# Performance work log

Hardware: AMD Instinct MI355X
Metric: run time of the kernel (lower is better)

## Reference

```python
import jax, jax.numpy as jnp
import numpy as np

T, B, D = 128, 64, 1024  # timesteps, batch, mem_dim (== in_dim)


def setup_inputs() -> dict:
    key = jax.random.key(0)
    ks = jax.random.split(key, 10)
    w = lambda k, shape: jax.random.normal(k, shape, dtype=jnp.float32) * 0.02
    return dict(
        c=jax.random.normal(ks[0], (T, B, D), dtype=jnp.float32),
        q=jax.random.normal(ks[1], (B, D), dtype=jnp.float32),
        Wb_w=w(ks[2], (D, D)),                 # nn.Linear(mem_dim, mem_dim, bias=False)
        W1_w=w(ks[3], (D, 9 * D)),             # nn.Linear(9*mem_dim, mem_dim)
        W1_b=jnp.zeros((D,), jnp.float32),
        W2_w=w(ks[4], (D, D)),                 # nn.Linear(mem_dim, mem_dim)
        W2_b=jnp.zeros((D,), jnp.float32),
        mem_Wih=w(ks[5], (3 * D, D)), mem_Whh=w(ks[6], (3 * D, D)),
        mem_bih=jnp.zeros((3 * D,), jnp.float32), mem_bhh=jnp.zeros((3 * D,), jnp.float32),
        att_Wih=w(ks[7], (3 * D, D)), att_Whh=w(ks[8], (3 * D, D)),
        att_bih=jnp.zeros((3 * D,), jnp.float32), att_bhh=jnp.zeros((3 * D,), jnp.float32),
    )


def gru_cell(x, h, Wih, Whh, bih, bhh):
    # torch.nn.GRUCell semantics
    gi = x @ Wih.T + bih  # [B, 3D]
    gh = h @ Whh.T + bhh  # [B, 3D]
    i_r, i_z, i_n = jnp.split(gi, 3, axis=-1)
    h_r, h_z, h_n = jnp.split(gh, 3, axis=-1)
    r = jax.nn.sigmoid(i_r + h_r)
    z = jax.nn.sigmoid(i_z + h_z)
    n = jnp.tanh(i_n + r * h_n)
    return (1.0 - z) * n + z * h


def reference(c, q, Wb_w, W1_w, W1_b, W2_w, W2_b,
              mem_Wih, mem_Whh, mem_bih, mem_bhh,
              att_Wih, att_Whh, att_bih, att_bhh):
    N_EPISODE = 2

    def episode(m):
        # Wb(q), Wb(m) are step-invariant -> hoist out of the scan
        Wbq = q @ Wb_w.T  # [B, D]
        Wbm = m @ Wb_w.T  # [B, D]

        def step(h, c_t):
            # make_z: 9-way feature concat -> [B, 9D]
            z = jnp.concatenate(
                [c_t, m, q, c_t * q, c_t * m,
                 jnp.abs(c_t - q), jnp.abs(c_t - m),
                 c_t * Wbq, c_t * Wbm], axis=-1)
            g1 = jnp.tanh(z @ W1_w.T + W1_b)            # [B, D]
            g = jax.nn.sigmoid(g1 @ W2_w.T + W2_b)      # [B, D]
            h_att = gru_cell(c_t, h, att_Wih, att_Whh, att_bih, att_bhh)
            h_new = g * h_att + (1.0 - g) * h
            return h_new, None

        h_T, _ = jax.lax.scan(step, jnp.zeros_like(m), c)
        return h_T

    m = q
    for _ in range(N_EPISODE):
        e = episode(m)
        m = gru_cell(e, m, mem_Wih, mem_Whh, mem_bih, mem_bhh)
    return m
```

## Files before the change

### kernel.cpp

```cpp
#include <hip/hip_runtime.h>


typedef unsigned short u16;
typedef unsigned long long u64;
typedef __attribute__((ext_vector_type(8))) short bf16x8;
typedef __attribute__((ext_vector_type(8))) unsigned short u16x8;
typedef __attribute__((ext_vector_type(4))) float f32x4;

__device__ inline float bf2f(u16 u) {
    union { unsigned u; float f; } v; v.u = ((unsigned)u) << 16; return v.f;
}
__device__ inline u16 f2bf(float f) {
    union { float f; unsigned u; } v; v.f = f;
    unsigned r = v.u + 0x7fff + ((v.u >> 16) & 1);
    return (u16)(r >> 16);
}
__device__ inline float sigf(float x) { return 1.f / (1.f + expf(-x)); }

__device__ inline u64 cload64(const u16* p) {
    return __hip_atomic_load((const u64*)p, __ATOMIC_RELAXED, __HIP_MEMORY_SCOPE_SYSTEM);
}
__device__ inline void cstore64(u16* p, u64 v) {
    __hip_atomic_store((u64*)p, v, __ATOMIC_RELAXED, __HIP_MEMORY_SCOPE_SYSTEM);
}

__global__ void fill_sentinel(float* __restrict__ d, int n, float v) {
    for (int i = blockIdx.x * 256 + threadIdx.x; i < n; i += gridDim.x * 256) d[i] = v;
}

__global__ void zero_state(u16* __restrict__ hb, unsigned* __restrict__ slots, int n) {
    int i = blockIdx.x * 256 + threadIdx.x;
    for (int j = i; j < n / 4; j += gridDim.x * 256)
        __hip_atomic_store((u64*)hb + j, 0ull, __ATOMIC_RELAXED, __HIP_MEMORY_SCOPE_SYSTEM);
    if (i < 1088)
        __hip_atomic_store(slots + i, 0u, __ATOMIC_RELAXED, __HIP_MEMORY_SCOPE_SYSTEM);
}

__global__ void conv_bf(const float* __restrict__ s, u16* __restrict__ d, int n) {
    for (int i = blockIdx.x * 256 + threadIdx.x; i < n; i += gridDim.x * 256)
        d[i] = f2bf(s[i]);
}

__global__ void repack_w1(const float* __restrict__ W1, u16* __restrict__ out) {
    const int jmap[9] = {0, 3, 5, 7, 4, 6, 8, 1, 2};
    const int total = 1024 * 9216;
    for (int i = blockIdx.x * 256 + threadIdx.x; i < total; i += gridDim.x * 256) {
        int n = i / 9216;
        int rest = i - n * 9216;
        int v = rest >> 10, k = rest & 1023;
        out[(size_t)n * 9216 + rest] = f2bf(W1[(size_t)n * 9216 + jmap[v] * 1024 + k]);
    }
}

__global__ void build_zq(const float* __restrict__ c, const float* __restrict__ q,
                         const float* __restrict__ wbq, u16* __restrict__ Zq) {
    const int total = 8192 * 1024;
    for (int i = blockIdx.x * 256 + threadIdx.x; i < total; i += gridDim.x * 256) {
        int row = i >> 10, k = i & 1023, b = row & 63;
        float cv = c[i];
        float qv = q[b * 1024 + k];
        float wv = wbq[b * 1024 + k];
        size_t ro = (size_t)row * 4096;
        Zq[ro + k]        = f2bf(cv);
        Zq[ro + 1024 + k] = f2bf(cv * qv);
        Zq[ro + 2048 + k] = f2bf(fabsf(cv - qv));
        Zq[ro + 3072 + k] = f2bf(cv * wv);
    }
}

__global__ void build_zm(const float* __restrict__ c, const float* __restrict__ m,
                         const float* __restrict__ wbm, u16* __restrict__ Zm) {
    const int total = 8192 * 1024;
    for (int i = blockIdx.x * 256 + threadIdx.x; i < total; i += gridDim.x * 256) {
        int row = i >> 10, k = i & 1023, b = row & 63;
        float cv = c[i];
        float mv = m[b * 1024 + k];
        float wv = wbm[b * 1024 + k];
        size_t ro = (size_t)row * 3072;
        Zm[ro + k]        = f2bf(cv * mv);
        Zm[ro + 1024 + k] = f2bf(fabsf(cv - mv));
        Zm[ro + 2048 + k] = f2bf(cv * wv);
    }
}

template <int MODE>
__global__ __launch_bounds__(256) void gemm_bt(
    const u16* __restrict__ A, int lda,
    const u16* __restrict__ B, int ldb,
    void* __restrict__ C, int M, int N, int K,
    const float* __restrict__ bias,
    const float* __restrict__ prevf,
    const float* __restrict__ addb) {
    __shared__ u16 As[128 * 40];
    __shared__ u16 Bs[128 * 40];
    const int t = threadIdx.x;
    const int bn = blockIdx.x, bm = blockIdx.y;
    const int w = t >> 6, lane = t & 63, lr = lane & 15, quad = lane >> 4;
    const int wm = (w >> 1) * 64, wn = (w & 1) * 64;
    const int r0 = t >> 2, kb = (t & 3) * 8;

    f32x4 zero4 = {0.f, 0.f, 0.f, 0.f};
    f32x4 acc[4][4];
#pragma unroll
    for (int i = 0; i < 4; i++)
#pragma unroll
        for (int j = 0; j < 4; j++) acc[i][j] = zero4;

    const u16x8 zz = {0, 0, 0, 0, 0, 0, 0, 0};

    for (int k0 = 0; k0 < K; k0 += 32) {
#pragma unroll
        for (int rr = r0; rr < 128; rr += 64) {
            int gm = bm * 128 + rr;
            u16x8 av = zz;
            if (gm < M) av = *(const u16x8*)(A + (size_t)gm * lda + k0 + kb);
            *(u16x8*)(As + rr * 40 + kb) = av;
            int gn = bn * 128 + rr;
            *(u16x8*)(Bs + rr * 40 + kb) = *(const u16x8*)(B + (size_t)gn * ldb + k0 + kb);
        }
        __syncthreads();
        bf16x8 af[4], bfr[4];
#pragma unroll
        for (int i = 0; i < 4; i++) af[i] = *(const bf16x8*)(As + (wm + i * 16 + lr) * 40 + quad * 8);
#pragma unroll
        for (int j = 0; j < 4; j++) bfr[j] = *(const bf16x8*)(Bs + (wn + j * 16 + lr) * 40 + quad * 8);
#pragma unroll
        for (int i = 0; i < 4; i++)
#pragma unroll
            for (int j = 0; j < 4; j++)
                acc[i][j] = __builtin_amdgcn_mfma_f32_16x16x32_bf16(af[i], bfr[j], acc[i][j], 0, 0, 0);
        __syncthreads();
    }

#pragma unroll
    for (int i = 0; i < 4; i++) {
        int gm0 = bm * 128 + wm + i * 16 + quad * 4;
#pragma unroll
        for (int j = 0; j < 4; j++) {
            int gn = bn * 128 + wn + j * 16 + lr;
#pragma unroll
            for (int reg = 0; reg < 4; reg++) {
                int gm = gm0 + reg;
                if (gm >= M) continue;
                float v = acc[i][j][reg];
                size_t o = (size_t)gm * N + gn;
                if constexpr (MODE == 0) ((float*)C)[o] = v;
                else if constexpr (MODE == 1) ((float*)C)[o] = v + bias[gn];
                else if constexpr (MODE == 2) ((u16*)C)[o] = f2bf(v + bias[gn]);
                else if constexpr (MODE == 3) ((float*)C)[o] = v + prevf[o];
                else if constexpr (MODE == 4)
                    ((u16*)C)[o] = f2bf(tanhf(v + prevf[o] + addb[(size_t)(gm & 63) * N + gn]));
                else if constexpr (MODE == 5) ((u16*)C)[o] = f2bf(sigf(v + bias[gn]));
            }
        }
    }
}

__global__ __launch_bounds__(256, 1) void gru_persist(
    const u16* __restrict__ Whh, const float* __restrict__ bhh,
    const u16* __restrict__ GIb, const u16* __restrict__ G,
    u16* __restrict__ hA, u16* __restrict__ hB,
    unsigned* __restrict__ slots) {
    extern __shared__ u16 Ws[];
    u16* hch = Ws + 48 * 1032;
    unsigned* goflag = slots + 1024;
    const int tid = threadIdx.x;
    const int bid = blockIdx.x;
    const int ds = bid * 16;
    const int w = tid >> 6, lane = tid & 63, lr = lane & 15, quad = lane >> 4;

    for (int idx = tid; idx < 48 * 128; idx += 256) {
        int r = idx >> 7, col8 = (idx & 127) * 8;
        int g = r >> 4, dl = r & 15;
        *(u16x8*)(Ws + r * 1032 + col8) =
            *(const u16x8*)(Whh + (size_t)(g * 1024 + ds + dl) * 1024 + col8);
    }

    const int b = w * 16 + lr;
    const int d0 = ds + quad * 4;
    f32x4 bhr4 = *(const f32x4*)(bhh + d0);
    f32x4 bhz4 = *(const f32x4*)(bhh + 1024 + d0);
    f32x4 bhn4 = *(const f32x4*)(bhh + 2048 + d0);
    f32x4 h = {0.f, 0.f, 0.f, 0.f};

    const u16* wsA = Ws + lr * 1032 + quad * 8;
    const u16* hrd = hch + (w * 16 + lr) * 264 + quad * 8;

    const int lrow[2] = {tid >> 5, (256 + tid) >> 5};
    __syncthreads();

    for (int t = 0; t < 128; t++) {
        const u16* hin = (t & 1) ? hB : hA;
        u16* hout = (t & 1) ? hA : hB;

        const u16* GIt = GIb + (size_t)t * 196608;
        const u16* Gt = G + (size_t)t * 65536;
        u64 pgir = *(const u64*)(GIt + b * 3072 + d0);
        u64 pgiz = *(const u64*)(GIt + b * 3072 + 1024 + d0);
        u64 pgin = *(const u64*)(GIt + b * 3072 + 2048 + d0);
        u64 pgg  = *(const u64*)(Gt + b * 1024 + d0);

        f32x4 accr = {0.f, 0.f, 0.f, 0.f}, accz = accr, accn = accr;

        u64 pf[16];
#pragma unroll
        for (int l = 0; l < 8; l++) {
            int u = l * 256 + tid;
            const u16* gp = hin + (u >> 5) * 1024 + (u & 31) * 8;
            pf[2 * l] = cload64(gp);
            pf[2 * l + 1] = cload64(gp + 4);
        }

        for (int c = 0; c < 4; c++) {
            __syncthreads();
#pragma unroll
            for (int l = 0; l < 8; l++) {
                int u = l * 256 + tid;
                union { u64 q[2]; u16x8 v; } pv;
                pv.q[0] = pf[2 * l]; pv.q[1] = pf[2 * l + 1];
                *(u16x8*)(hch + (u >> 5) * 264 + (u & 31) * 8) = pv.v;
            }
            __syncthreads();
            if (c < 3) {
#pragma unroll
                for (int l = 0; l < 8; l++) {
                    int u = l * 256 + tid;
                    const u16* gp = hin + (u >> 5) * 1024 + (c + 1) * 256 + (u & 31) * 8;
                    pf[2 * l] = cload64(gp);
                    pf[2 * l + 1] = cload64(gp + 4);
                }
            }
#pragma unroll
            for (int ki = 0; ki < 8; ki++) {
                int kl = ki * 32;
                int kg = c * 256 + kl;
                bf16x8 bv = *(const bf16x8*)(hrd + kl);
                bf16x8 a_r = *(const bf16x8*)(wsA + kg);
                bf16x8 a_z = *(const bf16x8*)(wsA + 16 * 1032 + kg);
                bf16x8 a_n = *(const bf16x8*)(wsA + 32 * 1032 + kg);
                accr = __builtin_amdgcn_mfma_f32_16x16x32_bf16(a_r, bv, accr, 0, 0, 0);
                accz = __builtin_amdgcn_mfma_f32_16x16x32_bf16(a_z, bv, accz, 0, 0, 0);
                accn = __builtin_amdgcn_mfma_f32_16x16x32_bf16(a_n, bv, accn, 0, 0, 0);
            }
        }

        u64 outv = 0;
#pragma unroll
        for (int reg = 0; reg < 4; reg++) {
            float r = sigf(bf2f((u16)(pgir >> (16 * reg))) + accr[reg] + bhr4[reg]);
            float z = sigf(bf2f((u16)(pgiz >> (16 * reg))) + accz[reg] + bhz4[reg]);
            float n = tanhf(bf2f((u16)(pgin >> (16 * reg))) + r * (accn[reg] + bhn4[reg]));
            float hatt = (1.f - z) * n + z * h[reg];
            float g = bf2f((u16)(pgg >> (16 * reg)));
            h[reg] = g * hatt + (1.f - g) * h[reg];
            outv |= (u64)f2bf(h[reg]) << (16 * reg);
        }
        cstore64(hout + b * 1024 + d0, outv);

        if (t == 127) break;

        unsigned epoch = (unsigned)(t + 1);
        __syncthreads();
        if (tid == 0)
            __hip_atomic_store(slots + bid * 16, epoch, __ATOMIC_RELAXED,
                               __HIP_MEMORY_SCOPE_SYSTEM);
        if (bid == 0) {
            if (tid < 64) {
                while (__hip_atomic_load(slots + tid * 16, __ATOMIC_RELAXED,
                                         __HIP_MEMORY_SCOPE_SYSTEM) < epoch)
                    __builtin_amdgcn_s_sleep(1);
            }
            __syncthreads();
            if (tid == 0)
                __hip_atomic_store(goflag, epoch, __ATOMIC_RELAXED,
                                   __HIP_MEMORY_SCOPE_SYSTEM);
        }
        if (tid == 0) {
            while (__hip_atomic_load(goflag, __ATOMIC_RELAXED,
                                     __HIP_MEMORY_SCOPE_SYSTEM) < epoch)
                __builtin_amdgcn_s_sleep(1);
        }
        __syncthreads();
    }
}

__global__ __launch_bounds__(256) void gru_mem(
    const u16* __restrict__ ebf, const u16* __restrict__ mbf,
    const float* __restrict__ mold,
    const u16* __restrict__ Wih, const u16* __restrict__ Whh,
    const float* __restrict__ bih, const float* __restrict__ bhh,
    float* __restrict__ mout, u16* __restrict__ mbf_out) {
    __shared__ u16 es[64 * 40];
    __shared__ u16 ms[64 * 40];
    __shared__ u16 Wi[192 * 40];
    __shared__ u16 Wh[192 * 40];
    const int t = threadIdx.x;
    const int ds = blockIdx.x * 64;
    const int w = t >> 6, lane = t & 63, lr = lane & 15, quad = lane >> 4;
    const int r0 = t >> 2, kb = (t & 3) * 8;

    f32x4 zero4 = {0.f, 0.f, 0.f, 0.f};
    f32x4 ai[4][3], ah[4][3];
#pragma unroll
    for (int i = 0; i < 4; i++)
#pragma unroll
        for (int g = 0; g < 3; g++) { ai[i][g] = zero4; ah[i][g] = zero4; }

    for (int k0 = 0; k0 < 1024; k0 += 32) {
        union { u64 q[2]; u16x8 v; } eu;
        eu.q[0] = cload64(ebf + r0 * 1024 + k0 + kb);
        eu.q[1] = cload64(ebf + r0 * 1024 + k0 + kb + 4);
        *(u16x8*)(es + r0 * 40 + kb) = eu.v;
        *(u16x8*)(ms + r0 * 40 + kb) = *(const u16x8*)(mbf + r0 * 1024 + k0 + kb);
#pragma unroll
        for (int ln = r0; ln < 192; ln += 64) {
            int g = ln >> 6, dl = ln & 63;
            size_t ro = (size_t)(g * 1024 + ds + dl) * 1024 + k0 + kb;
            *(u16x8*)(Wi + ln * 40 + kb) = *(const u16x8*)(Wih + ro);
            *(u16x8*)(Wh + ln * 40 + kb) = *(const u16x8*)(Whh + ro);
        }
        __syncthreads();
        bf16x8 ae[4], am[4], bi[3], bh[3];
#pragma unroll
        for (int i = 0; i < 4; i++) {
            ae[i] = *(const bf16x8*)(es + (i * 16 + lr) * 40 + quad * 8);
            am[i] = *(const bf16x8*)(ms + (i * 16 + lr) * 40 + quad * 8);
        }
#pragma unroll
        for (int g = 0; g < 3; g++) {
            bi[g] = *(const bf16x8*)(Wi + (g * 64 + w * 16 + lr) * 40 + quad * 8);
            bh[g] = *(const bf16x8*)(Wh + (g * 64 + w * 16 + lr) * 40 + quad * 8);
        }
#pragma unroll
        for (int i = 0; i < 4; i++)
#pragma unroll
            for (int g = 0; g < 3; g++) {
                ai[i][g] = __builtin_amdgcn_mfma_f32_16x16x32_bf16(ae[i], bi[g], ai[i][g], 0, 0, 0);
                ah[i][g] = __builtin_amdgcn_mfma_f32_16x16x32_bf16(am[i], bh[g], ah[i][g], 0, 0, 0);
            }
        __syncthreads();
    }

    const int d = ds + w * 16 + lr;
    const float bir = bih[d], biz = bih[1024 + d], bin = bih[2048 + d];
    const float bhr = bhh[d], bhz = bhh[1024 + d], bhn = bhh[2048 + d];
#pragma unroll
    for (int i = 0; i < 4; i++) {
#pragma unroll
        for (int reg = 0; reg < 4; reg++) {
            int b = i * 16 + quad * 4 + reg;
            float r = sigf(ai[i][0][reg] + bir + ah[i][0][reg] + bhr);
            float z = sigf(ai[i][1][reg] + biz + ah[i][1][reg] + bhz);
            float n = tanhf(ai[i][2][reg] + bin + r * (ah[i][2][reg] + bhn));
            float mo = mold[b * 1024 + d];
            float mn = (1.f - z) * n + z * mo;
            mout[b * 1024 + d] = mn;
            mbf_out[b * 1024 + d] = f2bf(mn);
        }
    }
}

extern "C" void kernel_launch(void* const* d_in, const int* in_sizes, int n_in,
                              void* d_out, int out_size, void* d_ws, size_t ws_size,
                              hipStream_t stream) {
    const float* c    = (const float*)d_in[0];
    const float* q    = (const float*)d_in[1];
    const float* Wb   = (const float*)d_in[2];
    const float* W1   = (const float*)d_in[3];
    const float* W1b  = (const float*)d_in[4];
    const float* W2   = (const float*)d_in[5];
    const float* W2b  = (const float*)d_in[6];
    const float* mWih = (const float*)d_in[7];
    const float* mWhh = (const float*)d_in[8];
    const float* mbih = (const float*)d_in[9];
    const float* mbhh = (const float*)d_in[10];
    const float* aWih = (const float*)d_in[11];
    const float* aWhh = (const float*)d_in[12];
    const float* abih = (const float*)d_in[13];
    const float* abhh = (const float*)d_in[14];

    char* p = (char*)d_ws;
    auto nb = [&](size_t bytes) -> char* {
        char* r = p; p += (bytes + 255) & ~(size_t)255; return r;
    };
    u16* W1p     = (u16*)nb(1024ull * 9216 * 2);
    u16* Wb_bf   = (u16*)nb(1024ull * 1024 * 2);
    u16* W2_bf   = (u16*)nb(1024ull * 1024 * 2);
    u16* aWih_bf = (u16*)nb(3072ull * 1024 * 2);
    u16* aWhh_bf = (u16*)nb(3072ull * 1024 * 2);
    u16* mWih_bf = (u16*)nb(3072ull * 1024 * 2);
    u16* mWhh_bf = (u16*)nb(3072ull * 1024 * 2);
    u16* qbf     = (u16*)nb(64 * 1024 * 2);
    u16* m1bf    = (u16*)nb(64 * 1024 * 2);
    u16* m2bf    = (u16*)nb(64 * 1024 * 2);
    u16* hA      = (u16*)nb(64 * 1024 * 2);
    u16* hB      = (u16*)nb(64 * 1024 * 2);
    u16* Zq      = (u16*)nb(8192ull * 4096 * 2);
    u16* GIb     = (u16*)nb(8192ull * 3072 * 2);
    u16* G1      = (u16*)nb(8192ull * 1024 * 2);
    u16* G       = (u16*)nb(8192ull * 1024 * 2);
    float* P0    = (float*)nb(8192ull * 1024 * 4);
    float* Wbq   = (float*)nb(64 * 1024 * 4);
    float* Wbm   = (float*)nb(64 * 1024 * 4);
    float* addq  = (float*)nb(64 * 1024 * 4);
    float* addt  = (float*)nb(64 * 1024 * 4);
    float* m1    = (float*)nb(64 * 1024 * 4);
    unsigned* slots = (unsigned*)nb(1088 * 4 + 256);
    u16* Zm      = Zq;

    size_t needed = (size_t)(p - (char*)d_ws);
    if (needed > ws_size) {
        fill_sentinel<<<256, 256, 0, stream>>>((float*)d_out, out_size, 12345.0f);
        return;
    }

    static bool attr_set = false;
    const int ws_lds = (48 * 1032 + 64 * 264) * 2;
    if (!attr_set) {
        (void)hipFuncSetAttribute((const void*)gru_persist,
                                  hipFuncAttributeMaxDynamicSharedMemorySize, ws_lds);
        attr_set = true;
    }

    conv_bf<<<256, 256, 0, stream>>>(q, qbf, 64 * 1024);
    conv_bf<<<2048, 256, 0, stream>>>(Wb, Wb_bf, 1024 * 1024);
    conv_bf<<<2048, 256, 0, stream>>>(W2, W2_bf, 1024 * 1024);
    conv_bf<<<4096, 256, 0, stream>>>(aWih, aWih_bf, 3072 * 1024);
    conv_bf<<<4096, 256, 0, stream>>>(aWhh, aWhh_bf, 3072 * 1024);
    conv_bf<<<4096, 256, 0, stream>>>(mWih, mWih_bf, 3072 * 1024);
    conv_bf<<<4096, 256, 0, stream>>>(mWhh, mWhh_bf, 3072 * 1024);
    repack_w1<<<8192, 256, 0, stream>>>(W1, W1p);

    gemm_bt<0><<<dim3(8, 1), 256, 0, stream>>>(qbf, 1024, Wb_bf, 1024, Wbq, 64, 1024, 1024,
                                               nullptr, nullptr, nullptr);
    gemm_bt<1><<<dim3(8, 1), 256, 0, stream>>>(qbf, 1024, W1p + 8192, 9216, addq, 64, 1024, 1024,
                                               W1b, nullptr, nullptr);
    build_zq<<<16384, 256, 0, stream>>>(c, q, Wbq, Zq);
    gemm_bt<0><<<dim3(8, 64), 256, 0, stream>>>(Zq, 4096, W1p, 9216, P0, 8192, 1024, 4096,
                                                nullptr, nullptr, nullptr);
    gemm_bt<2><<<dim3(24, 64), 256, 0, stream>>>(Zq, 4096, aWih_bf, 1024, GIb, 8192, 3072, 1024,
                                                 abih, nullptr, nullptr);

    for (int ep = 0; ep < 2; ep++) {
        const u16* mbf_cur = ep ? m1bf : qbf;
        const float* mold  = ep ? (const float*)m1 : q;
        gemm_bt<3><<<dim3(8, 1), 256, 0, stream>>>(mbf_cur, 1024, W1p + 7168, 9216, addt,
                                                   64, 1024, 1024, nullptr, addq, nullptr);
        const u16* AG1; int ldaG1;
        if (ep) {
            gemm_bt<0><<<dim3(8, 1), 256, 0, stream>>>(m1bf, 1024, Wb_bf, 1024, Wbm,
                                                       64, 1024, 1024, nullptr, nullptr, nullptr);
            build_zm<<<16384, 256, 0, stream>>>(c, m1, Wbm, Zm);
            AG1 = Zm; ldaG1 = 3072;
        } else {
            AG1 = Zq + 1024; ldaG1 = 4096;
        }
        gemm_bt<4><<<dim3(8, 64), 256, 0, stream>>>(AG1, ldaG1, W1p + 4096, 9216, G1,
                                                    8192, 1024, 3072, nullptr, P0, addt);
        gemm_bt<5><<<dim3(8, 64), 256, 0, stream>>>(G1, 1024, W2_bf, 1024, G,
                                                    8192, 1024, 1024, W2b, nullptr, nullptr);

        zero_state<<<64, 256, 0, stream>>>(hA, slots, 64 * 1024);
        gru_persist<<<64, 256, ws_lds, stream>>>(aWhh_bf, abhh, GIb, G, hA, hB, slots);

        float* mo = ep ? (float*)d_out : m1;
        u16* mob = ep ? m2bf : m1bf;
        gru_mem<<<16, 256, 0, stream>>>(hA, mbf_cur, mold, mWih_bf, mWhh_bf,
                                        mbih, mbhh, mo, mob);
    }
}
```

Baseline: 2.873 ms.

## Replace centralized grid barrier with per-chunk producer flag waits in GRU scan

The persistent GRU kernel no longer runs a two-phase grid barrier (all blocks signal block 0, which then releases a go flag) after each timestep. Each block now publishes its own epoch flag, and before loading each 256-column chunk of h it waits only on the 16 producer blocks that write that chunk. A second prefetch buffer lets chunk loads run further ahead. This removes one round of global flag latency per step and lets blocks start on ready chunks early, in exchange for more polling traffic and more registers. Ordering still relies on relaxed atomics.

```diff
diff --git a/kernel.cpp b/kernel.cpp
--- a/kernel.cpp
+++ b/kernel.cpp
@@ -163,7 +163,6 @@
     unsigned* __restrict__ slots) {
     extern __shared__ u16 Ws[];
     u16* hch = Ws + 48 * 1032;
-    unsigned* goflag = slots + 1024;
     const int tid = threadIdx.x;
     const int bid = blockIdx.x;
     const int ds = bid * 16;
@@ -186,7 +185,11 @@
     const u16* wsA = Ws + lr * 1032 + quad * 8;
     const u16* hrd = hch + (w * 16 + lr) * 264 + quad * 8;
 
-    const int lrow[2] = {tid >> 5, (256 + tid) >> 5};
+    const int hrow0 = tid >> 5;
+    const int hcol = (tid & 31) * 8;
+    const int pofs = (tid & 31) >> 1;
+    const unsigned* psl = slots + (unsigned)(lane & 15) * 16;
+
     __syncthreads();
 
     for (int t = 0; t < 128; t++) {
@@ -200,35 +203,47 @@
         u64 pgin = *(const u64*)(GIt + b * 3072 + 2048 + d0);
         u64 pgg  = *(const u64*)(Gt + b * 1024 + d0);
 
+        const unsigned epoch = (unsigned)t;
+        u64 pf[2][16];
+
+        auto wait_chunk = [&](int c) {
+            const unsigned* sp = psl + c * 256;
+            for (;;) {
+                unsigned v = __hip_atomic_load(sp, __ATOMIC_RELAXED,
+                                               __HIP_MEMORY_SCOPE_SYSTEM);
+                if (__all(v >= epoch)) break;
+                __builtin_amdgcn_s_sleep(1);
+            }
+        };
+        auto issue_chunk = [&](int c, u64* dst) {
+            const u16* base = hin + c * 256 + hcol;
+#pragma unroll
+            for (int l = 0; l < 8; l++) {
+                const u16* gp = base + (l * 8 + hrow0) * 1024;
+                dst[2 * l] = cload64(gp);
+                dst[2 * l + 1] = cload64(gp + 4);
+            }
+        };
+
+        if (t > 0) wait_chunk(0);
+        issue_chunk(0, pf[0]);
+        if (t > 0) wait_chunk(1);
+        issue_chunk(1, pf[1]);
+
         f32x4 accr = {0.f, 0.f, 0.f, 0.f}, accz = accr, accn = accr;
-
-        u64 pf[16];
-#pragma unroll
-        for (int l = 0; l < 8; l++) {
-            int u = l * 256 + tid;
-            const u16* gp = hin + (u >> 5) * 1024 + (u & 31) * 8;
-            pf[2 * l] = cload64(gp);
-            pf[2 * l + 1] = cload64(gp + 4);
-        }
 
         for (int c = 0; c < 4; c++) {
             __syncthreads();
 #pragma unroll
             for (int l = 0; l < 8; l++) {
-                int u = l * 256 + tid;
                 union { u64 q[2]; u16x8 v; } pv;
-                pv.q[0] = pf[2 * l]; pv.q[1] = pf[2 * l + 1];
-                *(u16x8*)(hch + (u >> 5) * 264 + (u & 31) * 8) = pv.v;
+                pv.q[0] = pf[c & 1][2 * l]; pv.q[1] = pf[c & 1][2 * l + 1];
+                *(u16x8*)(hch + (l * 8 + hrow0) * 264 + hcol) = pv.v;
             }
             __syncthreads();
-            if (c < 3) {
-#pragma unroll
-                for (int l = 0; l < 8; l++) {
-                    int u = l * 256 + tid;
-                    const u16* gp = hin + (u >> 5) * 1024 + (c + 1) * 256 + (u & 31) * 8;
-                    pf[2 * l] = cload64(gp);
-                    pf[2 * l + 1] = cload64(gp + 4);
-                }
+            if (c < 2) {
+                if (t > 0) wait_chunk(c + 2);
+                issue_chunk(c + 2, pf[c & 1]);
             }
 #pragma unroll
             for (int ki = 0; ki < 8; ki++) {
@@ -257,30 +272,10 @@
         }
         cstore64(hout + b * 1024 + d0, outv);
 
-        if (t == 127) break;
-
-        unsigned epoch = (unsigned)(t + 1);
         __syncthreads();
-        if (tid == 0)
-            __hip_atomic_store(slots + bid * 16, epoch, __ATOMIC_RELAXED,
-                               __HIP_MEMORY_SCOPE_SYSTEM);
-        if (bid == 0) {
-            if (tid < 64) {
-                while (__hip_atomic_load(slots + tid * 16, __ATOMIC_RELAXED,
-                                         __HIP_MEMORY_SCOPE_SYSTEM) < epoch)
-                    __builtin_amdgcn_s_sleep(1);
-            }
-            __syncthreads();
-            if (tid == 0)
-                __hip_atomic_store(goflag, epoch, __ATOMIC_RELAXED,
-                                   __HIP_MEMORY_SCOPE_SYSTEM);
-        }
-        if (tid == 0) {
-            while (__hip_atomic_load(goflag, __ATOMIC_RELAXED,
-                                     __HIP_MEMORY_SCOPE_SYSTEM) < epoch)
-                __builtin_amdgcn_s_sleep(1);
-        }
-        __syncthreads();
+        if (tid == 0 && t < 127)
+            __hip_atomic_store(slots + bid * 16, (unsigned)(t + 1),
+                               __ATOMIC_RELAXED, __HIP_MEMORY_SCOPE_SYSTEM);
     }
 }
 
```

Result: slower. 3.003 ms (+4.5%).
